# Kernel tuning notes

Hardware: AMD Instinct MI355X
Metric: run time of the kernel (lower is better)

The kernel has to match this reference:

```python
import jax, jax.numpy as jnp
import numpy as np

N = 50000       # num nodes
E = 400000      # num edges (before self loops)
IN, HID, H, OUT = 128, 64, 4, 64
SLOPE = 0.2     # PyG GATv2Conv default negative_slope


def setup_inputs() -> dict:
    key = jax.random.key(0)
    ks = jax.random.split(key, 14)
    def lin(k, fan_in, fan_out):
        return jax.random.normal(k, (fan_in, fan_out), jnp.float32) / np.sqrt(fan_in)
    return {
        "x": jax.random.normal(ks[0], (N, IN), jnp.float32),
        "edge_index": jax.random.randint(ks[1], (2, E), 0, N, jnp.int32),
        # layer 1: in=IN -> HID per head, H heads, concat
        "Wl1": lin(ks[2], IN, H * HID), "bl1": jnp.zeros((H * HID,), jnp.float32),
        "Wr1": lin(ks[3], IN, H * HID), "br1": jnp.zeros((H * HID,), jnp.float32),
        "att1": jax.random.normal(ks[4], (H, HID), jnp.float32) / np.sqrt(HID),
        "bias1": jnp.zeros((H * HID,), jnp.float32),
        # layer 2: in=H*HID -> OUT, 1 head, concat=False
        "Wl2": lin(ks[5], H * HID, OUT), "bl2": jnp.zeros((OUT,), jnp.float32),
        "Wr2": lin(ks[6], H * HID, OUT), "br2": jnp.zeros((OUT,), jnp.float32),
        "att2": jax.random.normal(ks[7], (1, OUT), jnp.float32) / np.sqrt(OUT),
        "bias2": jnp.zeros((OUT,), jnp.float32),
    }


def gatv2_conv(x, src, dst, Wl, bl, Wr, br, att, heads, out_ch, num_nodes):
    """PyG GATv2Conv (share_weights=False). src->dst aggregation at dst."""
    xl = (x @ Wl + bl).reshape(-1, heads, out_ch)  # source transform (x_j)
    xr = (x @ Wr + br).reshape(-1, heads, out_ch)  # target transform (x_i)
    m = xl[src] + xr[dst]                          # [E, H, C]
    e = jnp.sum(jax.nn.leaky_relu(m, SLOPE) * att, axis=-1)  # [E, H]
    # segment softmax over incoming edges of each dst node
    emax = jax.ops.segment_max(e, dst, num_segments=num_nodes)
    ex = jnp.exp(e - emax[dst])
    denom = jax.ops.segment_sum(ex, dst, num_segments=num_nodes)
    alpha = ex / denom[dst]                        # [E, H]
    out = jax.ops.segment_sum(alpha[:, :, None] * xl[src], dst, num_segments=num_nodes)
    return out  # [N, H, C]


def reference(x, edge_index, Wl1, bl1, Wr1, br1, att1, bias1,
              Wl2, bl2, Wr2, br2, att2, bias2):
    n = x.shape[0]
    loops = jnp.arange(n, dtype=edge_index.dtype)
    src = jnp.concatenate([edge_index[0], loops])  # add_self_loops=True
    dst = jnp.concatenate([edge_index[1], loops])
    h = gatv2_conv(x, src, dst, Wl1, bl1, Wr1, br1, att1, H, HID, n)
    h = h.reshape(n, H * HID) + bias1              # concat=True
    h = jax.nn.elu(h)                              # dropout=0.0
    o = gatv2_conv(h, src, dst, Wl2, bl2, Wr2, br2, att2, 1, OUT, n)
    return o.reshape(n, OUT) + bias2               # concat=False, heads=1
```

## Files before the change

kernel.cpp:

```cpp
#include <hip/hip_runtime.h>
#include <hip/hip_bf16.h>

typedef unsigned short u16;
typedef __attribute__((ext_vector_type(8))) short short8;
typedef __attribute__((ext_vector_type(4))) float floatx4;
typedef __attribute__((ext_vector_type(2))) float f32x2;

#define N_NODES 50000
#define N_EDGES 400000
#define ET      450000
#define F_IN    128
#define C1      256
#define HID     64
#define OUTC    64
#define SLOPE   0.2f

__device__ __forceinline__ float bf2f(u16 v) {
    return __uint_as_float(((unsigned)v) << 16);
}
__device__ __forceinline__ float bflo(unsigned u) { return __uint_as_float(u << 16); }
__device__ __forceinline__ float bfhi(unsigned u) { return __uint_as_float(u & 0xffff0000u); }
__device__ __forceinline__ u16 f2bf(float f) {
    unsigned u = __float_as_uint(f);
    return (u16)((u + 0x7fffu + ((u >> 16) & 1u)) >> 16);
}
__device__ __forceinline__ f32x2 up2(unsigned u) {
    f32x2 r; r.x = bflo(u); r.y = bfhi(u); return r;
}
template<int CTRL>
__device__ __forceinline__ float dpp_add(float x) {
    return x + __int_as_float(__builtin_amdgcn_update_dpp(
        0, __float_as_int(x), CTRL, 0xF, 0xF, true));
}
__device__ __forceinline__ float red16(float p) {
    p = dpp_add<0xB1>(p);
    p = dpp_add<0x4E>(p);
    p = dpp_add<0x141>(p);
    p = dpp_add<0x140>(p);
    return p;
}
__device__ __forceinline__ bool detect_f32(const unsigned* __restrict__ xw) {
    unsigned w = xw[threadIdx.x & 63];
    unsigned aexp = (w >> 7) & 0xFFu;
    unsigned long long b = __ballot(aexp >= 170u || aexp <= 40u);
    return __popcll(b) >= 16;
}

__global__ __launch_bounds__(256) void convert_all_kernel(
    const unsigned* __restrict__ xw,
    const void* wl1, const void* wr1, const void* wl2, const void* wr2,
    const void* s0, const void* s1, const void* s2, const void* s3,
    const void* s4, const void* s5, const void* s6, const void* s7,
    u16* __restrict__ wt, u16* __restrict__ prm, int* __restrict__ hist)
{
    if (blockIdx.x >= 385) {
        int idx = (blockIdx.x - 385) * 256 + threadIdx.x;
        if (idx < N_NODES) hist[idx] = 0;
        return;
    }
    bool f32m = detect_f32(xw);
    if (blockIdx.x == 384) {
        for (int t = threadIdx.x; t < 1280; t += 256) {
            const void* src; int local;
            if      (t < 256)  { src = s0; local = t; }
            else if (t < 512)  { src = s1; local = t - 256; }
            else if (t < 768)  { src = s2; local = t - 512; }
            else if (t < 1024) { src = s3; local = t - 768; }
            else if (t < 1088) { src = s4; local = t - 1024; }
            else if (t < 1152) { src = s5; local = t - 1088; }
            else if (t < 1216) { src = s6; local = t - 1152; }
            else               { src = s7; local = t - 1216; }
            prm[t] = f32m ? f2bf(((const float*)src)[local]) : ((const u16*)src)[local];
        }
        return;
    }
    int t = blockIdx.x * 256 + threadIdx.x;
    const void* src; int local, k, n, K, base;
    if (t < 32768)      { src = wl1; local = t;         k = local >> 8; n = local & 255; K = 128; base = 0; }
    else if (t < 65536) { src = wr1; local = t - 32768; k = local >> 8; n = local & 255; K = 128; base = 32768; }
    else if (t < 81920) { src = wl2; local = t - 65536; k = local >> 6; n = local & 63;  K = 256; base = 65536; }
    else                { src = wr2; local = t - 81920; k = local >> 6; n = local & 63;  K = 256; base = 81920; }
    u16 v = f32m ? f2bf(((const float*)src)[local]) : ((const u16*)src)[local];
    wt[base + n * K + k] = v;
}

__global__ __launch_bounds__(256) void hist_kernel(const int* __restrict__ ei,
                                                   int* __restrict__ hist)
{
    int t = blockIdx.x * 256 + threadIdx.x;
    if (t >= ET) return;
    int d = (t < N_EDGES) ? ei[N_EDGES + t] : t - N_EDGES;
    atomicAdd(&hist[d], 1);
}

__global__ __launch_bounds__(256) void scan1_kernel(const int* __restrict__ hist,
                                                    int* __restrict__ rowptr,
                                                    int* __restrict__ bsum)
{
    int t = threadIdx.x;
    int i = blockIdx.x * 256 + t;
    int v = (i < N_NODES) ? hist[i] : 0;
    __shared__ int sd[256];
    sd[t] = v;
    __syncthreads();
    #pragma unroll
    for (int ofs = 1; ofs < 256; ofs <<= 1) {
        int u = (t >= ofs) ? sd[t - ofs] : 0;
        __syncthreads();
        sd[t] += u;
        __syncthreads();
    }
    if (i < N_NODES) rowptr[i] = sd[t] - v;
    if (t == 255) bsum[blockIdx.x] = sd[255];
}

__global__ __launch_bounds__(256) void scan3_kernel(int* __restrict__ rowptr,
                                                    const int* __restrict__ bsum,
                                                    int* __restrict__ off)
{
    int t = threadIdx.x;
    int v = (t < (int)blockIdx.x) ? bsum[t] : 0;
    __shared__ int sd[256];
    sd[t] = v;
    __syncthreads();
    #pragma unroll
    for (int ofs = 1; ofs < 256; ofs <<= 1) {
        int u = (t >= ofs) ? sd[t - ofs] : 0;
        __syncthreads();
        sd[t] += u;
        __syncthreads();
    }
    int boff = sd[255];
    int i = blockIdx.x * 256 + t;
    if (i < N_NODES) {
        int r = rowptr[i] + boff;
        rowptr[i] = r;
        off[i] = r;
    }
}

__global__ __launch_bounds__(256) void scatter_kernel(const int* __restrict__ ei,
                                                      int* __restrict__ off,
                                                      int* __restrict__ src_csr)
{
    int t = blockIdx.x * 256 + threadIdx.x;
    if (t >= ET) return;
    int s, d;
    if (t < N_EDGES) { s = ei[t]; d = ei[N_EDGES + t]; } else { s = d = t - N_EDGES; }
    int pos = atomicAdd(&off[d], 1);
    src_csr[pos] = s;
}

__global__ __launch_bounds__(256) void lin1_fused_kernel(
    const u16* __restrict__ X, const u16* __restrict__ Wt,
    const u16* __restrict__ bl, const u16* __restrict__ br,
    u16* __restrict__ Yl, u16* __restrict__ Yr, int nrows)
{
    constexpr int K = 128, N = 256, LS = K + 8;
    __shared__ __align__(16) u16 sX[64 * LS];
    __shared__ __align__(16) u16 sW[64 * LS];
    const bool f32m = detect_f32((const unsigned*)X);
    const float* X32 = (const float*)X;
    const int row0 = blockIdx.x * 64;
    const int wave = threadIdx.x >> 6, lane = threadIdx.x & 63;
    const int quad = lane >> 4, l16 = lane & 15;

    for (int i = threadIdx.x * 8; i < 64 * K; i += 2048) {
        int r = i >> 7, c = i & 127;
        int gr = row0 + r;
        u16* dst = &sX[r * LS + c];
        if (f32m) {
            float4 v0 = make_float4(0.f, 0.f, 0.f, 0.f), v1 = v0;
            if (gr < nrows) {
                v0 = *(const float4*)&X32[(size_t)gr * K + c];
                v1 = *(const float4*)&X32[(size_t)gr * K + c + 4];
            }
            ushort4 p0, p1;
            p0.x = f2bf(v0.x); p0.y = f2bf(v0.y); p0.z = f2bf(v0.z); p0.w = f2bf(v0.w);
            p1.x = f2bf(v1.x); p1.y = f2bf(v1.y); p1.z = f2bf(v1.z); p1.w = f2bf(v1.w);
            *(ushort4*)dst = p0;
            *(ushort4*)(dst + 4) = p1;
        } else {
            uint4 v = {0u, 0u, 0u, 0u};
            if (gr < nrows) v = *(const uint4*)&X[(size_t)gr * K + c];
            *(uint4*)dst = v;
        }
    }
    __syncthreads();

    short8 a[4];
    #pragma unroll
    for (int kk = 0; kk < 4; ++kk)
        a[kk] = *(const short8*)&sX[(wave * 16 + l16) * LS + kk * 32 + quad * 8];

    for (int side = 0; side < 2; ++side) {
        const u16* wbase = Wt + side * (N * K);
        const u16* bias  = side ? br : bl;
        u16* Y = side ? Yr : Yl;
        for (int ch = 0; ch < 4; ++ch) {
            __syncthreads();
            for (int i = threadIdx.x * 8; i < 64 * K; i += 2048) {
                int n = i >> 7, c = i & 127;
                *(uint4*)&sW[n * LS + c] = *(const uint4*)&wbase[(size_t)(ch * 64 + n) * K + c];
            }
            __syncthreads();
            floatx4 acc0 = {0.f, 0.f, 0.f, 0.f}, acc1 = acc0, acc2 = acc0, acc3 = acc0;
            #pragma unroll
            for (int kk = 0; kk < 4; ++kk) {
                short8 b0 = *(const short8*)&sW[(l16) * LS + kk * 32 + quad * 8];
                short8 b1 = *(const short8*)&sW[(16 + l16) * LS + kk * 32 + quad * 8];
                short8 b2 = *(const short8*)&sW[(32 + l16) * LS + kk * 32 + quad * 8];
                short8 b3 = *(const short8*)&sW[(48 + l16) * LS + kk * 32 + quad * 8];
                acc0 = __builtin_amdgcn_mfma_f32_16x16x32_bf16(a[kk], b0, acc0, 0, 0, 0);
                acc1 = __builtin_amdgcn_mfma_f32_16x16x32_bf16(a[kk], b1, acc1, 0, 0, 0);
                acc2 = __builtin_amdgcn_mfma_f32_16x16x32_bf16(a[kk], b2, acc2, 0, 0, 0);
                acc3 = __builtin_amdgcn_mfma_f32_16x16x32_bf16(a[kk], b3, acc3, 0, 0, 0);
            }
            const int rbase = row0 + wave * 16 + quad * 4;
            #pragma unroll
            for (int cf = 0; cf < 4; ++cf) {
                const floatx4 av = (cf == 0) ? acc0 : (cf == 1) ? acc1 : (cf == 2) ? acc2 : acc3;
                const int col = ch * 64 + cf * 16 + l16;
                const float bv = bf2f(bias[col]);
                #pragma unroll
                for (int r = 0; r < 4; ++r) {
                    int row = rbase + r;
                    if (row < nrows) Y[(size_t)row * N + col] = f2bf(av[r] + bv);
                }
            }
        }
    }
}

__global__ __launch_bounds__(256) void lin2_fused_kernel(
    const u16* __restrict__ X, const u16* __restrict__ Wt,
    const u16* __restrict__ bl, const u16* __restrict__ br,
    u16* __restrict__ Yl, u16* __restrict__ Yr, int nrows)
{
    constexpr int K = 256, N = 64, LS = K + 8;
    __shared__ __align__(16) u16 sX[64 * LS];
    __shared__ __align__(16) u16 sW[64 * LS];
    const int row0 = blockIdx.x * 64;
    const int wave = threadIdx.x >> 6, lane = threadIdx.x & 63;
    const int quad = lane >> 4, l16 = lane & 15;

    for (int i = threadIdx.x * 8; i < 64 * K; i += 2048) {
        int r = i >> 8, c = i & 255;
        int gr = row0 + r;
        uint4 v = {0u, 0u, 0u, 0u};
        if (gr < nrows) v = *(const uint4*)&X[(size_t)gr * K + c];
        *(uint4*)&sX[r * LS + c] = v;
    }
    __syncthreads();

    short8 a[8];
    #pragma unroll
    for (int kk = 0; kk < 8; ++kk)
        a[kk] = *(const short8*)&sX[(wave * 16 + l16) * LS + kk * 32 + quad * 8];

    for (int side = 0; side < 2; ++side) {
        const u16* wbase = Wt + side * (N * K);
        const u16* bias  = side ? br : bl;
        u16* Y = side ? Yr : Yl;
        __syncthreads();
        for (int i = threadIdx.x * 8; i < 64 * K; i += 2048) {
            int n = i >> 8, c = i & 255;
            *(uint4*)&sW[n * LS + c] = *(const uint4*)&wbase[(size_t)n * K + c];
        }
        __syncthreads();
        floatx4 acc0 = {0.f, 0.f, 0.f, 0.f}, acc1 = acc0, acc2 = acc0, acc3 = acc0;
        #pragma unroll
        for (int kk = 0; kk < 8; ++kk) {
            short8 b0 = *(const short8*)&sW[(l16) * LS + kk * 32 + quad * 8];
            short8 b1 = *(const short8*)&sW[(16 + l16) * LS + kk * 32 + quad * 8];
            short8 b2 = *(const short8*)&sW[(32 + l16) * LS + kk * 32 + quad * 8];
            short8 b3 = *(const short8*)&sW[(48 + l16) * LS + kk * 32 + quad * 8];
            acc0 = __builtin_amdgcn_mfma_f32_16x16x32_bf16(a[kk], b0, acc0, 0, 0, 0);
            acc1 = __builtin_amdgcn_mfma_f32_16x16x32_bf16(a[kk], b1, acc1, 0, 0, 0);
            acc2 = __builtin_amdgcn_mfma_f32_16x16x32_bf16(a[kk], b2, acc2, 0, 0, 0);
            acc3 = __builtin_amdgcn_mfma_f32_16x16x32_bf16(a[kk], b3, acc3, 0, 0, 0);
        }
        const int rbase = row0 + wave * 16 + quad * 4;
        #pragma unroll
        for (int cf = 0; cf < 4; ++cf) {
            const floatx4 av = (cf == 0) ? acc0 : (cf == 1) ? acc1 : (cf == 2) ? acc2 : acc3;
            const int col = cf * 16 + l16;
            const float bv = bf2f(bias[col]);
            #pragma unroll
            for (int r = 0; r < 4; ++r) {
                int row = rbase + r;
                if (row < nrows) Y[(size_t)row * N + col] = f2bf(av[r] + bv);
            }
        }
    }
}

__global__ __launch_bounds__(256) void node1_kernel(
    const u16* __restrict__ xl, const u16* __restrict__ xr,
    const int* __restrict__ rowptr, const int* __restrict__ hist,
    const int* __restrict__ src_csr, const u16* __restrict__ att,
    const u16* __restrict__ bias, u16* __restrict__ hout, int d0)
{
    const int d = __builtin_amdgcn_readfirstlane(d0 + blockIdx.x * 4 + (threadIdx.x >> 6));
    if (d >= N_NODES) return;
    const int l = threadIdx.x & 63;
    const int start = rowptr[d];
    const int deg = hist[d];

    uint2 auv = *(const uint2*)&att[l * 4];
    const f32x2 atA = up2(auv.x), atB = up2(auv.y);
    uint2 ruv = *(const uint2*)&xr[(size_t)d * C1 + l * 4];
    const f32x2 rA = up2(ruv.x), rB = up2(ruv.y);

    float m = -1e30f, la = 0.f;
    f32x2 accA = {0.f, 0.f}, accB = {0.f, 0.f};
    for (int j = 0; j < deg; j += 4) {
        const bool v1 = j + 1 < deg, v2 = j + 2 < deg, v3 = j + 3 < deg;
        int s0 = src_csr[start + j];
        int s1 = v1 ? src_csr[start + j + 1] : s0;
        int s2 = v2 ? src_csr[start + j + 2] : s0;
        int s3 = v3 ? src_csr[start + j + 3] : s0;
        uint2 u0 = *(const uint2*)&xl[(size_t)s0 * C1 + l * 4];
        uint2 u1 = *(const uint2*)&xl[(size_t)s1 * C1 + l * 4];
        uint2 u2 = *(const uint2*)&xl[(size_t)s2 * C1 + l * 4];
        uint2 u3 = *(const uint2*)&xl[(size_t)s3 * C1 + l * 4];
        f32x2 x0A = up2(u0.x), x0B = up2(u0.y);
        f32x2 x1A = up2(u1.x), x1B = up2(u1.y);
        f32x2 x2A = up2(u2.x), x2B = up2(u2.y);
        f32x2 x3A = up2(u3.x), x3B = up2(u3.y);
        f32x2 t, pv;
        t = x0A + rA; t = __builtin_elementwise_max(t, t * SLOPE); pv  = t * atA;
        t = x0B + rB; t = __builtin_elementwise_max(t, t * SLOPE); pv += t * atB;
        float p0 = pv.x + pv.y;
        t = x1A + rA; t = __builtin_elementwise_max(t, t * SLOPE); pv  = t * atA;
        t = x1B + rB; t = __builtin_elementwise_max(t, t * SLOPE); pv += t * atB;
        float p1 = pv.x + pv.y;
        t = x2A + rA; t = __builtin_elementwise_max(t, t * SLOPE); pv  = t * atA;
        t = x2B + rB; t = __builtin_elementwise_max(t, t * SLOPE); pv += t * atB;
        float p2 = pv.x + pv.y;
        t = x3A + rA; t = __builtin_elementwise_max(t, t * SLOPE); pv  = t * atA;
        t = x3B + rB; t = __builtin_elementwise_max(t, t * SLOPE); pv += t * atB;
        float p3 = pv.x + pv.y;
        p0 = red16(p0); p1 = red16(p1); p2 = red16(p2); p3 = red16(p3);
        float pm = p0;
        if (v1) pm = fmaxf(pm, p1);
        if (v2) pm = fmaxf(pm, p2);
        if (v3) pm = fmaxf(pm, p3);
        float mn = fmaxf(m, pm);
        float sc = __expf(m - mn);
        float w0 = __expf(p0 - mn);
        float w1 = v1 ? __expf(p1 - mn) : 0.f;
        float w2 = v2 ? __expf(p2 - mn) : 0.f;
        float w3 = v3 ? __expf(p3 - mn) : 0.f;
        la = la * sc + w0 + w1 + w2 + w3;
        accA = accA * sc + x0A * w0 + x1A * w1 + x2A * w2 + x3A * w3;
        accB = accB * sc + x0B * w0 + x1B * w1 + x2B * w2 + x3B * w3;
        m = mn;
    }
    const float inv = 1.f / la;
    const int c = l * 4;
    float v0 = accA.x * inv + bf2f(bias[c + 0]);
    float v1 = accA.y * inv + bf2f(bias[c + 1]);
    float v2 = accB.x * inv + bf2f(bias[c + 2]);
    float v3 = accB.y * inv + bf2f(bias[c + 3]);
    v0 = v0 > 0.f ? v0 : __expf(fminf(v0, 0.f)) - 1.f;
    v1 = v1 > 0.f ? v1 : __expf(fminf(v1, 0.f)) - 1.f;
    v2 = v2 > 0.f ? v2 : __expf(fminf(v2, 0.f)) - 1.f;
    v3 = v3 > 0.f ? v3 : __expf(fminf(v3, 0.f)) - 1.f;
    ushort4 o;
    o.x = f2bf(v0); o.y = f2bf(v1); o.z = f2bf(v2); o.w = f2bf(v3);
    *(ushort4*)&hout[(size_t)d * C1 + c] = o;
}

__global__ __launch_bounds__(256) void node2_kernel(
    const u16* __restrict__ xl, const u16* __restrict__ xr,
    const int* __restrict__ rowptr, const int* __restrict__ hist,
    const int* __restrict__ src_csr, const u16* __restrict__ att,
    const u16* __restrict__ bias, void* __restrict__ outp,
    const unsigned* __restrict__ xorig)
{
    const bool f32o = detect_f32(xorig);
    const int d = __builtin_amdgcn_readfirstlane(blockIdx.x * 4 + (threadIdx.x >> 6));
    if (d >= N_NODES) return;
    const int l = threadIdx.x & 63;
    const int start = rowptr[d];
    const int deg = hist[d];
    const int g = l >> 4, sub = l & 15;
    const int c0 = sub * 4;

    uint2 auv = *(const uint2*)&att[c0];
    const f32x2 atA = up2(auv.x), atB = up2(auv.y);
    uint2 ruv = *(const uint2*)&xr[(size_t)d * OUTC + c0];
    const f32x2 rA = up2(ruv.x), rB = up2(ruv.y);

    float m = -1e30f, la = 0.f;
    f32x2 accA = {0.f, 0.f}, accB = {0.f, 0.f};
    for (int j = 0; j < deg; j += 4) {
        const bool valid = j + g < deg;
        int s = valid ? src_csr[start + j + g] : d;
        uint2 uv = *(const uint2*)&xl[(size_t)s * OUTC + c0];
        f32x2 xA = up2(uv.x), xB = up2(uv.y);
        f32x2 t, pv;
        t = xA + rA; t = __builtin_elementwise_max(t, t * SLOPE); pv  = t * atA;
        t = xB + rB; t = __builtin_elementwise_max(t, t * SLOPE); pv += t * atB;
        float p = pv.x + pv.y;
        p = red16(p);
        float pvv = valid ? p : -1e30f;
        float mn = fmaxf(m, pvv);
        float sc = __expf(m - mn);
        float w  = valid ? __expf(p - mn) : 0.f;
        la = la * sc + w;
        accA = accA * sc + xA * w;
        accB = accB * sc + xB * w;
        m = mn;
    }
    #pragma unroll
    for (int ofs = 16; ofs <= 32; ofs <<= 1) {
        float mo = __shfl_xor(m, ofs);
        float lo = __shfl_xor(la, ofs);
        float bax = __shfl_xor(accA.x, ofs);
        float bay = __shfl_xor(accA.y, ofs);
        float bbx = __shfl_xor(accB.x, ofs);
        float bby = __shfl_xor(accB.y, ofs);
        float mn = fmaxf(m, mo);
        float s0 = __expf(m - mn), s1 = __expf(mo - mn);
        la = la * s0 + lo * s1;
        accA.x = accA.x * s0 + bax * s1;
        accA.y = accA.y * s0 + bay * s1;
        accB.x = accB.x * s0 + bbx * s1;
        accB.y = accB.y * s0 + bby * s1;
        m = mn;
    }
    if (g == 0) {
        const float inv = 1.f / la;
        float v0 = accA.x * inv + bf2f(bias[c0 + 0]);
        float v1 = accA.y * inv + bf2f(bias[c0 + 1]);
        float v2 = accB.x * inv + bf2f(bias[c0 + 2]);
        float v3 = accB.y * inv + bf2f(bias[c0 + 3]);
        if (f32o) {
            float4 o = make_float4(v0, v1, v2, v3);
            *(float4*)&((float*)outp)[(size_t)d * OUTC + c0] = o;
        } else {
            ushort4 o;
            o.x = f2bf(v0); o.y = f2bf(v1); o.z = f2bf(v2); o.w = f2bf(v3);
            *(ushort4*)&((u16*)outp)[(size_t)d * OUTC + c0] = o;
        }
    }
}

extern "C" void kernel_launch(void* const* d_in, const int* in_sizes, int n_in,
                              void* d_out, int out_size, void* d_ws, size_t ws_size,
                              hipStream_t stream)
{
    const void* x  = d_in[0];
    const int*  ei = (const int*)d_in[1];

    char* ws = (char*)d_ws;
    u16* xl1     = (u16*)(ws + 0);
    u16* xr1     = (u16*)(ws + 25600000);
    u16* hbuf    = (u16*)(ws + 51200000);
    u16* xl2     = (u16*)(ws + 0);
    u16* xr2     = (u16*)(ws + 6400000);
    int* hist    = (int*)(ws + 76800000);
    int* rowptr  = (int*)(ws + 77000000);
    int* off     = (int*)(ws + 77200000);
    int* src_csr = (int*)(ws + 77400000);
    u16* prm     = (u16*)(ws + 79200064);
    u16* wt      = (u16*)(ws + 79210240);
    int* bsum    = (int*)(ws + 79410000);

    u16* bl1   = prm + 0;
    u16* br1   = prm + 256;
    u16* att1  = prm + 512;
    u16* bias1 = prm + 768;
    u16* bl2   = prm + 1024;
    u16* br2   = prm + 1088;
    u16* att2  = prm + 1152;
    u16* bias2 = prm + 1216;
    u16* wt1   = wt + 0;
    u16* wt2   = wt + 65536;

    convert_all_kernel<<<581, 256, 0, stream>>>(
        (const unsigned*)x,
        d_in[2], d_in[4], d_in[8], d_in[10],
        d_in[3], d_in[5], d_in[6], d_in[7], d_in[9], d_in[11], d_in[12], d_in[13],
        wt, prm, hist);

    const int eb = (ET + 255) / 256;
    hist_kernel<<<eb, 256, 0, stream>>>(ei, hist);
    scan1_kernel<<<196, 256, 0, stream>>>(hist, rowptr, bsum);
    scan3_kernel<<<196, 256, 0, stream>>>(rowptr, bsum, off);
    scatter_kernel<<<eb, 256, 0, stream>>>(ei, off, src_csr);

    const int gb = (N_NODES + 63) / 64;
    lin1_fused_kernel<<<gb, 256, 0, stream>>>((const u16*)x, wt1, bl1, br1, xl1, xr1, N_NODES);
    const int nbh = 6250;
    node1_kernel<<<nbh, 256, 0, stream>>>(xl1, xr1, rowptr, hist, src_csr, att1, bias1, hbuf, 0);
    node1_kernel<<<nbh, 256, 0, stream>>>(xl1, xr1, rowptr, hist, src_csr, att1, bias1, hbuf, 25000);
    lin2_fused_kernel<<<gb, 256, 0, stream>>>(hbuf, wt2, bl2, br2, xl2, xr2, N_NODES);
    node2_kernel<<<(N_NODES * 64 + 255) / 256, 256, 0, stream>>>(
        xl2, xr2, rowptr, hist, src_csr, att2, bias2, d_out, (const unsigned*)x);
}
```

Measured before the change: 266.2 us.

## Fuse degree histogram into lin1 kernel, double lin1 row tile, merge node1 launches

The edge-degree histogram work becomes extra blocks of the layer-1 linear kernel, so the atomics run alongside the GEMM and one launch is dropped. The lin1 tile grows from 64 to 128 rows per block, so each staged weight chunk feeds twice as many MFMAs, at the cost of more LDS and registers. The two half-range node1 launches are merged into a single launch over all nodes. This trades launch overhead and weight reloads for lower occupancy in lin1 and a mix of atomic-heavy and MFMA blocks in one grid.

```diff
diff --git a/kernel.cpp b/kernel.cpp
--- a/kernel.cpp
+++ b/kernel.cpp
@@ -14,6 +14,7 @@
 #define HID     64
 #define OUTC    64
 #define SLOPE   0.2f
+#define LIN1_BLOCKS 391
 
 __device__ __forceinline__ float bf2f(u16 v) {
     return __uint_as_float(((unsigned)v) << 16);
@@ -84,15 +85,6 @@
     wt[base + n * K + k] = v;
 }
 
-__global__ __launch_bounds__(256) void hist_kernel(const int* __restrict__ ei,
-                                                   int* __restrict__ hist)
-{
-    int t = blockIdx.x * 256 + threadIdx.x;
-    if (t >= ET) return;
-    int d = (t < N_EDGES) ? ei[N_EDGES + t] : t - N_EDGES;
-    atomicAdd(&hist[d], 1);
-}
-
 __global__ __launch_bounds__(256) void scan1_kernel(const int* __restrict__ hist,
                                                     int* __restrict__ rowptr,
                                                     int* __restrict__ bsum)
@@ -151,21 +143,32 @@
     src_csr[pos] = s;
 }
 
-__global__ __launch_bounds__(256) void lin1_fused_kernel(
+__global__ __launch_bounds__(256) void lin1_hist_kernel(
     const u16* __restrict__ X, const u16* __restrict__ Wt,
     const u16* __restrict__ bl, const u16* __restrict__ br,
-    u16* __restrict__ Yl, u16* __restrict__ Yr, int nrows)
+    u16* __restrict__ Yl, u16* __restrict__ Yr, int nrows,
+    const int* __restrict__ ei, int* __restrict__ hist)
 {
     constexpr int K = 128, N = 256, LS = K + 8;
-    __shared__ __align__(16) u16 sX[64 * LS];
+    __shared__ __align__(16) u16 sX[128 * LS];
     __shared__ __align__(16) u16 sW[64 * LS];
+
+    if (blockIdx.x >= LIN1_BLOCKS) {
+        int t = (blockIdx.x - LIN1_BLOCKS) * 256 + threadIdx.x;
+        if (t < ET) {
+            int d = (t < N_EDGES) ? ei[N_EDGES + t] : t - N_EDGES;
+            atomicAdd(&hist[d], 1);
+        }
+        return;
+    }
+
     const bool f32m = detect_f32((const unsigned*)X);
     const float* X32 = (const float*)X;
-    const int row0 = blockIdx.x * 64;
+    const int row0 = blockIdx.x * 128;
     const int wave = threadIdx.x >> 6, lane = threadIdx.x & 63;
     const int quad = lane >> 4, l16 = lane & 15;
 
-    for (int i = threadIdx.x * 8; i < 64 * K; i += 2048) {
+    for (int i = threadIdx.x * 8; i < 128 * K; i += 2048) {
         int r = i >> 7, c = i & 127;
         int gr = row0 + r;
         u16* dst = &sX[r * LS + c];
@@ -188,10 +191,12 @@
     }
     __syncthreads();
 
-    short8 a[4];
+    short8 a0[4], a1[4];
     #pragma unroll
-    for (int kk = 0; kk < 4; ++kk)
-        a[kk] = *(const short8*)&sX[(wave * 16 + l16) * LS + kk * 32 + quad * 8];
+    for (int kk = 0; kk < 4; ++kk) {
+        a0[kk] = *(const short8*)&sX[(wave * 16 + l16) * LS + kk * 32 + quad * 8];
+        a1[kk] = *(const short8*)&sX[(64 + wave * 16 + l16) * LS + kk * 32 + quad * 8];
+    }
 
     for (int side = 0; side < 2; ++side) {
         const u16* wbase = Wt + side * (N * K);
@@ -204,28 +209,36 @@
                 *(uint4*)&sW[n * LS + c] = *(const uint4*)&wbase[(size_t)(ch * 64 + n) * K + c];
             }
             __syncthreads();
-            floatx4 acc0 = {0.f, 0.f, 0.f, 0.f}, acc1 = acc0, acc2 = acc0, acc3 = acc0;
+            floatx4 p0 = {0.f, 0.f, 0.f, 0.f}, p1 = p0, p2 = p0, p3 = p0;
+            floatx4 q0 = p0, q1 = p0, q2 = p0, q3 = p0;
             #pragma unroll
             for (int kk = 0; kk < 4; ++kk) {
                 short8 b0 = *(const short8*)&sW[(l16) * LS + kk * 32 + quad * 8];
                 short8 b1 = *(const short8*)&sW[(16 + l16) * LS + kk * 32 + quad * 8];
                 short8 b2 = *(const short8*)&sW[(32 + l16) * LS + kk * 32 + quad * 8];
                 short8 b3 = *(const short8*)&sW[(48 + l16) * LS + kk * 32 + quad * 8];
-                acc0 = __builtin_amdgcn_mfma_f32_16x16x32_bf16(a[kk], b0, acc0, 0, 0, 0);
-                acc1 = __builtin_amdgcn_mfma_f32_16x16x32_bf16(a[kk], b1, acc1, 0, 0, 0);
-                acc2 = __builtin_amdgcn_mfma_f32_16x16x32_bf16(a[kk], b2, acc2, 0, 0, 0);
-                acc3 = __builtin_amdgcn_mfma_f32_16x16x32_bf16(a[kk], b3, acc3, 0, 0, 0);
+                p0 = __builtin_amdgcn_mfma_f32_16x16x32_bf16(a0[kk], b0, p0, 0, 0, 0);
+                p1 = __builtin_amdgcn_mfma_f32_16x16x32_bf16(a0[kk], b1, p1, 0, 0, 0);
+                p2 = __builtin_amdgcn_mfma_f32_16x16x32_bf16(a0[kk], b2, p2, 0, 0, 0);
+                p3 = __builtin_amdgcn_mfma_f32_16x16x32_bf16(a0[kk], b3, p3, 0, 0, 0);
+                q0 = __builtin_amdgcn_mfma_f32_16x16x32_bf16(a1[kk], b0, q0, 0, 0, 0);
+                q1 = __builtin_amdgcn_mfma_f32_16x16x32_bf16(a1[kk], b1, q1, 0, 0, 0);
+                q2 = __builtin_amdgcn_mfma_f32_16x16x32_bf16(a1[kk], b2, q2, 0, 0, 0);
+                q3 = __builtin_amdgcn_mfma_f32_16x16x32_bf16(a1[kk], b3, q3, 0, 0, 0);
             }
-            const int rbase = row0 + wave * 16 + quad * 4;
+            const int rb0 = row0 + wave * 16 + quad * 4;
             #pragma unroll
             for (int cf = 0; cf < 4; ++cf) {
-                const floatx4 av = (cf == 0) ? acc0 : (cf == 1) ? acc1 : (cf == 2) ? acc2 : acc3;
+                const floatx4 av = (cf == 0) ? p0 : (cf == 1) ? p1 : (cf == 2) ? p2 : p3;
+                const floatx4 bw = (cf == 0) ? q0 : (cf == 1) ? q1 : (cf == 2) ? q2 : q3;
                 const int col = ch * 64 + cf * 16 + l16;
                 const float bv = bf2f(bias[col]);
                 #pragma unroll
                 for (int r = 0; r < 4; ++r) {
-                    int row = rbase + r;
-                    if (row < nrows) Y[(size_t)row * N + col] = f2bf(av[r] + bv);
+                    int rowA = rb0 + r;
+                    if (rowA < nrows) Y[(size_t)rowA * N + col] = f2bf(av[r] + bv);
+                    int rowB = rowA + 64;
+                    if (rowB < nrows) Y[(size_t)rowB * N + col] = f2bf(bw[r] + bv);
                 }
             }
         }
@@ -299,9 +312,9 @@
     const u16* __restrict__ xl, const u16* __restrict__ xr,
     const int* __restrict__ rowptr, const int* __restrict__ hist,
     const int* __restrict__ src_csr, const u16* __restrict__ att,
-    const u16* __restrict__ bias, u16* __restrict__ hout, int d0)
-{
-    const int d = __builtin_amdgcn_readfirstlane(d0 + blockIdx.x * 4 + (threadIdx.x >> 6));
+    const u16* __restrict__ bias, u16* __restrict__ hout)
+{
+    const int d = __builtin_amdgcn_readfirstlane(blockIdx.x * 4 + (threadIdx.x >> 6));
     if (d >= N_NODES) return;
     const int l = threadIdx.x & 63;
     const int start = rowptr[d];
@@ -487,17 +500,16 @@
         wt, prm, hist);
 
     const int eb = (ET + 255) / 256;
-    hist_kernel<<<eb, 256, 0, stream>>>(ei, hist);
+    lin1_hist_kernel<<<LIN1_BLOCKS + eb, 256, 0, stream>>>(
+        (const u16*)x, wt1, bl1, br1, xl1, xr1, N_NODES, ei, hist);
+
     scan1_kernel<<<196, 256, 0, stream>>>(hist, rowptr, bsum);
     scan3_kernel<<<196, 256, 0, stream>>>(rowptr, bsum, off);
     scatter_kernel<<<eb, 256, 0, stream>>>(ei, off, src_csr);
 
-    const int gb = (N_NODES + 63) / 64;
-    lin1_fused_kernel<<<gb, 256, 0, stream>>>((const u16*)x, wt1, bl1, br1, xl1, xr1, N_NODES);
-    const int nbh = 6250;
-    node1_kernel<<<nbh, 256, 0, stream>>>(xl1, xr1, rowptr, hist, src_csr, att1, bias1, hbuf, 0);
-    node1_kernel<<<nbh, 256, 0, stream>>>(xl1, xr1, rowptr, hist, src_csr, att1, bias1, hbuf, 25000);
-    lin2_fused_kernel<<<gb, 256, 0, stream>>>(hbuf, wt2, bl2, br2, xl2, xr2, N_NODES);
-    node2_kernel<<<(N_NODES * 64 + 255) / 256, 256, 0, stream>>>(
-        xl2, xr2, rowptr, hist, src_csr, att2, bias2, d_out, (const unsigned*)x);
-}
+    const int nb = (N_NODES * 64 + 255) / 256;
+    node1_kernel<<<nb, 256, 0, stream>>>(xl1, xr1, rowptr, hist, src_csr, att1, bias1, hbuf);
+    lin2_fused_kernel<<<(N_NODES + 63) / 64, 256, 0, stream>>>(hbuf, wt2, bl2, br2, xl2, xr2, N_NODES);
+    node2_kernel<<<nb, 256, 0, stream>>>(xl2, xr2, rowptr, hist, src_csr, att2, bias2, d_out,
+                                         (const unsigned*)x);
+}
```

New measurement: 251.7 us. 1.06x faster.
